# Kernel optimization log

Hardware: AMD Instinct MI355X
Metric: run time of the kernel (lower is better)

Reference implementation:

```python
import jax, jax.numpy as jnp
import numpy as np

B, N, C, HEADS, R = 8, 4096, 256, 8, 4  # N = H*W, R = reduction_ratio
LN_EPS = 1e-5


def setup_inputs() -> dict:
    key = jax.random.key(0)
    ks = jax.random.split(key, 6)
    sc = 0.02
    return {
        "x": jax.random.normal(ks[0], (B, N, C), jnp.float32),
        "conv_w": jax.random.normal(ks[1], (C, C, R, R), jnp.float32) * sc,  # OIHW
        "conv_b": jnp.zeros((C,), jnp.float32),
        "ln_g": jnp.ones((C,), jnp.float32),
        "ln_b": jnp.zeros((C,), jnp.float32),
        "kv_w": jax.random.normal(ks[2], (2 * C, C), jnp.float32) * sc,  # torch Linear (out,in)
        "kv_b": jnp.zeros((2 * C,), jnp.float32),
        "q_w": jax.random.normal(ks[3], (C, C), jnp.float32) * sc,
        "q_b": jnp.zeros((C,), jnp.float32),
        "out_w": jax.random.normal(ks[4], (C, C), jnp.float32) * sc,
        "out_b": jnp.zeros((C,), jnp.float32),
        "H": 64,
        "W": 64,
    }


def reference(x, conv_w, conv_b, ln_g, ln_b, kv_w, kv_b, q_w, q_b, out_w, out_b, H, W):
    Bz, Nq, Ch = x.shape
    d = Ch // HEADS
    scale = 1.0 / np.sqrt(float(d)).astype(np.float32)

    # spatial reduction: (B,N,C) -> (B,C,H,W) -> strided conv -> (B, M, C)
    x1 = x.transpose(0, 2, 1).reshape(Bz, Ch, H, W)
    x1 = jax.lax.conv_general_dilated(
        x1, conv_w, window_strides=(R, R), padding="VALID",
        dimension_numbers=("NCHW", "OIHW", "NCHW"))
    x1 = x1 + conv_b[None, :, None, None]
    x1 = x1.reshape(Bz, Ch, -1).transpose(0, 2, 1)  # (B, M, C), M=(H/R)*(W/R)

    # LayerNorm over channels
    mu = x1.mean(-1, keepdims=True)
    var = x1.var(-1, keepdims=True)
    x1 = (x1 - mu) / jnp.sqrt(var + LN_EPS) * ln_g + ln_b

    # K,V from reduced tokens
    kv = x1 @ kv_w.T + kv_b                                  # (B, M, 2C)
    M = kv.shape[1]
    kv = kv.reshape(Bz, M, 2, HEADS, d).transpose(2, 0, 3, 1, 4)  # (2,B,h,M,d)
    k, v = kv[0], kv[1]

    # Q from full-resolution tokens
    q = (x @ q_w.T + q_b).reshape(Bz, Nq, HEADS, d).transpose(0, 2, 1, 3)  # (B,h,N,d)

    attn = jax.nn.softmax(jnp.einsum("bhnd,bhmd->bhnm", q, k) * scale, axis=-1)
    out = jnp.einsum("bhnm,bhmd->bhnd", attn, v)             # (B,h,N,d)
    out = out.transpose(0, 2, 1, 3).reshape(Bz, Nq, Ch)
    return out @ out_w.T + out_b
```

## Files before the change

kernel.cpp:

```cpp
#include <hip/hip_runtime.h>
#include <math.h>

#define LN_EPS 1e-5f
#define SCALE_QK 0.17677669529663687f

using bf16x8 = __bf16 __attribute__((ext_vector_type(8)));
using f32x4 = float __attribute__((ext_vector_type(4)));

__device__ __forceinline__ ushort f2bf(float f) {
  unsigned u = __float_as_uint(f);
  u += 0x7fff + ((u >> 16) & 1);
  return (ushort)(u >> 16);
}

__device__ __forceinline__ void gload_lds16(const ushort* g, ushort* l) {
  __builtin_amdgcn_global_load_lds((__attribute__((address_space(1))) void*)g,
                                   (__attribute__((address_space(3))) void*)l, 16, 0, 0);
}

__global__ __launch_bounds__(256) void prep_kernel(
    const float* __restrict__ x, ushort* __restrict__ xb,
    const float* __restrict__ qw, const float* __restrict__ kvw,
    const float* __restrict__ ow, const float* __restrict__ cw,
    ushort* __restrict__ qwb, ushort* __restrict__ kvwb,
    ushort* __restrict__ owb, ushort* __restrict__ wTb) {
  int blk = blockIdx.x, tid = threadIdx.x;
  if (blk < 2048) {
    int i = blk * 1024 + tid;
#pragma unroll
    for (int p = 0; p < 4; ++p) {
      float4 v = ((const float4*)x)[i + p * 256];
      ushort4 o = {f2bf(v.x), f2bf(v.y), f2bf(v.z), f2bf(v.w)};
      ((ushort4*)xb)[i + p * 256] = o;
    }
  } else if (blk < 2304) {
    int b2 = blk - 2048;
    const float* src;
    ushort* dst;
    int i;
    if (b2 < 64) { src = qw; dst = qwb; i = b2 * 256 + tid; }
    else if (b2 < 192) { src = kvw; dst = kvwb; i = (b2 - 64) * 256 + tid; }
    else { src = ow; dst = owb; i = (b2 - 192) * 256 + tid; }
    float4 v = ((const float4*)src)[i];
    ushort4 o = {f2bf(v.x), f2bf(v.y), f2bf(v.z), f2bf(v.w)};
    ((ushort4*)dst)[i] = o;
  } else {
    int oc = blk - 2304, ic = tid;
    const float* src = cw + (size_t)oc * 4096 + ic * 16;
#pragma unroll
    for (int pos = 0; pos < 16; ++pos)
      wTb[(size_t)oc * 4096 + pos * 256 + ic] = f2bf(src[pos]);
  }
}

template <bool CONV, bool BIAS, int OUTMODE>
__global__ __launch_bounds__(256) void mfma_gemm(const ushort* __restrict__ A,
                                                 const ushort* __restrict__ Bw,
                                                 const float* __restrict__ bias,
                                                 float* __restrict__ C,
                                                 ushort* __restrict__ aux,
                                                 ushort* __restrict__ aux2, int Kld,
                                                 int Kslice, int Nld, size_t zstride) {
  __shared__ __attribute__((aligned(16))) ushort As[128 * 32];
  __shared__ __attribute__((aligned(16))) ushort Bs[64 * 32];
  int tid = threadIdx.x;
  int lane = tid & 63, w = tid >> 6;
  int m0 = blockIdx.y * 128, n0 = blockIdx.x * 64;
  int kbase = blockIdx.z * Kslice;
  int arow0 = w * 16 + (lane >> 2);
  int acol = (lane & 3) * 8;
  f32x4 acc[2][4];
#pragma unroll
  for (int i = 0; i < 2; ++i)
#pragma unroll
    for (int j = 0; j < 4; ++j) acc[i][j] = (f32x4){0.f, 0.f, 0.f, 0.f};

  for (int k0 = 0; k0 < Kslice; k0 += 32) {
    int kg = kbase + k0;
    __syncthreads();
#pragma unroll
    for (int t = 0; t < 2; ++t) {
      int row = arow0 + t * 64;
      const ushort* src;
      if (CONV) {
        int m = m0 + row;
        int b = m >> 8, mm = m & 255;
        int oh = mm >> 4, ow = mm & 15;
        int k = kg + acol;
        int pos = k >> 8, ic = k & 255;
        int n = ((oh << 2) + (pos >> 2)) * 64 + (ow << 2) + (pos & 3);
        src = A + ((size_t)(b * 4096 + n) * 256 + ic);
      } else {
        src = A + ((size_t)(m0 + row) * Kld + kg + acol);
      }
      gload_lds16(src, &As[t * 2048 + w * 512]);
    }
    {
      const ushort* srcb = Bw + ((size_t)(n0 + w * 16 + (lane >> 2)) * Kld + kg + acol);
      gload_lds16(srcb, &Bs[w * 512]);
    }
    __syncthreads();
    int qk = (lane >> 4) * 8, l15 = lane & 15;
    bf16x8 a0 = *(const bf16x8*)&As[(w * 32 + l15) * 32 + qk];
    bf16x8 a1 = *(const bf16x8*)&As[(w * 32 + 16 + l15) * 32 + qk];
#pragma unroll
    for (int j = 0; j < 4; ++j) {
      bf16x8 bj = *(const bf16x8*)&Bs[(j * 16 + l15) * 32 + qk];
      acc[0][j] = __builtin_amdgcn_mfma_f32_16x16x32_bf16(a0, bj, acc[0][j], 0, 0, 0);
      acc[1][j] = __builtin_amdgcn_mfma_f32_16x16x32_bf16(a1, bj, acc[1][j], 0, 0, 0);
    }
  }
  int l15 = lane & 15, q = lane >> 4;
  if (OUTMODE == 0) {
    float* Cz = C + (size_t)blockIdx.z * zstride;
#pragma unroll
    for (int i = 0; i < 2; ++i) {
#pragma unroll
      for (int j = 0; j < 4; ++j) {
        int col = n0 + j * 16 + l15;
        float bv = BIAS ? bias[col] : 0.f;
#pragma unroll
        for (int r = 0; r < 4; ++r) {
          int row = m0 + w * 32 + i * 16 + q * 4 + r;
          Cz[(size_t)row * Nld + col] = acc[i][j][r] + bv;
        }
      }
    }
  } else {
#pragma unroll
    for (int i = 0; i < 2; ++i) {
      int rowb = m0 + w * 32 + i * 16 + q * 4;
      int b = rowb >> 8, mloc = rowb & 255;
#pragma unroll
      for (int j = 0; j < 4; ++j) {
        int col = n0 + j * 16 + l15;
        float bv = bias[col];
        if (col < 256) {
#pragma unroll
          for (int r = 0; r < 4; ++r)
            aux[(size_t)(b * 256 + mloc + r) * 256 + col] = f2bf(acc[i][j][r] + bv);
        } else {
          int c2 = col - 256, h = c2 >> 5, d = c2 & 31;
          unsigned lo = (unsigned)f2bf(acc[i][j][0] + bv) |
                        ((unsigned)f2bf(acc[i][j][1] + bv) << 16);
          unsigned hi = (unsigned)f2bf(acc[i][j][2] + bv) |
                        ((unsigned)f2bf(acc[i][j][3] + bv) << 16);
          *(uint2*)(aux2 + ((size_t)((b * 8 + h) * 32 + d) * 256 + mloc)) =
              make_uint2(lo, hi);
        }
      }
    }
  }
}

template <bool F32OUT>
__global__ __launch_bounds__(256, 2) void breg_gemm(const ushort* __restrict__ A,
                                                    const ushort* __restrict__ Bw,
                                                    const float* __restrict__ bias,
                                                    float* __restrict__ Cf,
                                                    ushort* __restrict__ Cb) {
  int tid = threadIdx.x, lane = tid & 63, w = tid >> 6;
  int l15 = lane & 15, quad = lane >> 4;
  int n0 = blockIdx.x * 64;
  int m0 = blockIdx.y * 256 + w * 64;
  bf16x8 bfr[4][8];
  const ushort* bbase = Bw + (size_t)(n0 + l15) * 256 + quad * 8;
#pragma unroll
  for (int j = 0; j < 4; ++j)
#pragma unroll
    for (int kc = 0; kc < 8; ++kc)
      bfr[j][kc] = *(const bf16x8*)(bbase + (size_t)j * 16 * 256 + kc * 32);
  float bv[4];
#pragma unroll
  for (int j = 0; j < 4; ++j) bv[j] = bias[n0 + j * 16 + l15];

#pragma unroll
  for (int t = 0; t < 4; ++t) {
    const ushort* arow = A + (size_t)(m0 + t * 16 + l15) * 256 + quad * 8;
    bf16x8 af[8];
#pragma unroll
    for (int kc = 0; kc < 8; ++kc) af[kc] = *(const bf16x8*)(arow + kc * 32);
    f32x4 acc[4];
#pragma unroll
    for (int j = 0; j < 4; ++j) acc[j] = (f32x4){0.f, 0.f, 0.f, 0.f};
#pragma unroll
    for (int kc = 0; kc < 8; ++kc)
#pragma unroll
      for (int j = 0; j < 4; ++j)
        acc[j] = __builtin_amdgcn_mfma_f32_16x16x32_bf16(af[kc], bfr[j][kc], acc[j], 0, 0, 0);
#pragma unroll
    for (int j = 0; j < 4; ++j)
#pragma unroll
      for (int r = 0; r < 4; ++r) {
        int row = m0 + t * 16 + quad * 4 + r;
        int col = n0 + j * 16 + l15;
        float vv = acc[j][r] + bv[j];
        if (F32OUT) Cf[(size_t)row * 256 + col] = vv;
        else Cb[(size_t)row * 256 + col] = f2bf(vv);
      }
  }
}

__global__ __launch_bounds__(256) void ln_fused(const float* __restrict__ part,
                                                const float* __restrict__ cb,
                                                const float* __restrict__ g,
                                                const float* __restrict__ bt,
                                                ushort* __restrict__ x1b) {
  int t = blockIdx.x, c = threadIdx.x;
  size_t idx = (size_t)t * 256 + c;
  float v = cb[c];
#pragma unroll
  for (int z = 0; z < 8; ++z) v += part[idx + (size_t)z * 524288];
  float s1 = v, s2 = v * v;
#pragma unroll
  for (int o = 32; o > 0; o >>= 1) {
    s1 += __shfl_down(s1, o, 64);
    s2 += __shfl_down(s2, o, 64);
  }
  __shared__ float r1[4], r2[4];
  __shared__ float mu_s, rstd_s;
  int wv = c >> 6, lane = c & 63;
  if (lane == 0) { r1[wv] = s1; r2[wv] = s2; }
  __syncthreads();
  if (c == 0) {
    float S1 = r1[0] + r1[1] + r1[2] + r1[3];
    float S2 = r2[0] + r2[1] + r2[2] + r2[3];
    float mu = S1 * (1.f / 256.f);
    float var = S2 * (1.f / 256.f) - mu * mu;
    mu_s = mu;
    rstd_s = rsqrtf(var + LN_EPS);
  }
  __syncthreads();
  x1b[idx] = f2bf((v - mu_s) * rstd_s * g[c] + bt[c]);
}

__global__ __launch_bounds__(256) void attn_mfma(const ushort* __restrict__ qbb,
                                                 const ushort* __restrict__ kb,
                                                 const ushort* __restrict__ vT,
                                                 ushort* __restrict__ aob) {
  __shared__ __attribute__((aligned(16))) ushort sh[4 * 16 * 264];
  int bid = blockIdx.x;
  int chunk = bid & 15, h = (bid >> 4) & 7, b = bid >> 7;
  int tid = threadIdx.x, lane = tid & 63, w = tid >> 6;
  int l15 = lane & 15, quad = lane >> 4;

  {
    const ushort* srcK = kb + (size_t)(b * 256 + w * 64 + (lane >> 2)) * 256 +
                         h * 32 + (lane & 3) * 8;
#pragma unroll
    for (int i = 0; i < 4; ++i)
      gload_lds16(srcK + (size_t)i * 16 * 256, &sh[(w * 64 + i * 16) * 32]);
    const ushort* srcV = vT + (size_t)((b * 8 + h) * 32 + w * 8 + (lane >> 5)) * 256 +
                         (lane & 31) * 8;
#pragma unroll
    for (int i = 0; i < 4; ++i)
      gload_lds16(srcV + (size_t)i * 2 * 256, &sh[8192 + (w * 8 + i * 2) * 256]);
  }
  __syncthreads();
  bf16x8 kf[16];
#pragma unroll
  for (int mt = 0; mt < 16; ++mt)
    kf[mt] = *(const bf16x8*)&sh[(mt * 16 + l15) * 32 + quad * 8];
  bf16x8 vf[2][8];
#pragma unroll
  for (int j = 0; j < 2; ++j)
#pragma unroll
    for (int kc = 0; kc < 8; ++kc)
      vf[j][kc] = *(const bf16x8*)&sh[8192 + (j * 16 + l15) * 256 + kc * 32 + quad * 8];
  __syncthreads();
  ushort* Pw = &sh[w * 16 * 264];

  const float Cc = SCALE_QK * 1.4426950408889634f;
  int q0base = b * 4096 + chunk * 256 + w * 64;

  for (int t = 0; t < 4; ++t) {
    int q0 = q0base + t * 16;
    bf16x8 qf = *(const bf16x8*)(qbb + (size_t)(q0 + l15) * 256 + h * 32 + quad * 8);
    float lsum = 0.f;
#pragma unroll
    for (int mt = 0; mt < 16; ++mt) {
      f32x4 st = __builtin_amdgcn_mfma_f32_16x16x32_bf16(
          kf[mt], qf, (f32x4){0.f, 0.f, 0.f, 0.f}, 0, 0, 0);
      unsigned u[4];
#pragma unroll
      for (int r = 0; r < 4; ++r) {
        float e = __builtin_amdgcn_exp2f(st[r] * Cc);
        lsum += e;
        u[r] = __float_as_uint(e) + 0x8000u;
      }
      unsigned lo = (u[0] >> 16) | (u[1] & 0xffff0000u);
      unsigned hi = (u[2] >> 16) | (u[3] & 0xffff0000u);
      *(uint2*)(Pw + l15 * 264 + mt * 16 + quad * 4) = make_uint2(lo, hi);
    }
    lsum += __shfl_xor(lsum, 16, 64);
    lsum += __shfl_xor(lsum, 32, 64);
    __builtin_amdgcn_s_waitcnt(0xc07f);
    f32x4 oacc[2] = {{0.f, 0.f, 0.f, 0.f}, {0.f, 0.f, 0.f, 0.f}};
#pragma unroll
    for (int kc = 0; kc < 8; ++kc) {
      bf16x8 pf = *(const bf16x8*)(Pw + l15 * 264 + kc * 32 + quad * 8);
      oacc[0] = __builtin_amdgcn_mfma_f32_16x16x32_bf16(pf, vf[0][kc], oacc[0], 0, 0, 0);
      oacc[1] = __builtin_amdgcn_mfma_f32_16x16x32_bf16(pf, vf[1][kc], oacc[1], 0, 0, 0);
    }
    float linv[4];
#pragma unroll
    for (int r = 0; r < 4; ++r) linv[r] = 1.0f / __shfl(lsum, quad * 4 + r, 64);
    ushort* ob = aob + (size_t)q0 * 256 + h * 32;
#pragma unroll
    for (int j = 0; j < 2; ++j)
#pragma unroll
      for (int r = 0; r < 4; ++r) {
        unsigned uo = __float_as_uint(oacc[j][r] * linv[r]) + 0x8000u;
        ob[(size_t)(quad * 4 + r) * 256 + j * 16 + l15] = (ushort)(uo >> 16);
      }
  }
}

extern "C" void kernel_launch(void* const* d_in, const int* in_sizes, int n_in,
                              void* d_out, int out_size, void* d_ws, size_t ws_size,
                              hipStream_t stream) {
  const float* x = (const float*)d_in[0];
  const float* conv_w = (const float*)d_in[1];
  const float* conv_b = (const float*)d_in[2];
  const float* ln_g = (const float*)d_in[3];
  const float* ln_b = (const float*)d_in[4];
  const float* kv_w = (const float*)d_in[5];
  const float* kv_b = (const float*)d_in[6];
  const float* q_w = (const float*)d_in[7];
  const float* q_b = (const float*)d_in[8];
  const float* out_w = (const float*)d_in[9];
  const float* out_b = (const float*)d_in[10];

  ushort* xb = (ushort*)d_ws;
  ushort* wTb = xb + 8388608;
  ushort* qwb = wTb + 1048576;
  ushort* kvwb = qwb + 65536;
  ushort* owb = kvwb + 131072;
  ushort* x1b = owb + 65536;
  ushort* kb = x1b + 524288;
  ushort* vT = kb + 524288;
  ushort* aob = xb;
  float* part = (float*)d_out;
  ushort* qbb = (ushort*)((float*)d_out + 4194304);

  prep_kernel<<<2560, 256, 0, stream>>>(x, xb, q_w, kv_w, out_w, conv_w,
                                        qwb, kvwb, owb, wTb);
  mfma_gemm<true, false, 0><<<dim3(4, 16, 8), 256, 0, stream>>>(
      xb, wTb, nullptr, part, nullptr, nullptr, 4096, 512, 256, 524288);
  ln_fused<<<2048, 256, 0, stream>>>(part, conv_b, ln_g, ln_b, x1b);
  mfma_gemm<false, true, 2><<<dim3(8, 16, 1), 256, 0, stream>>>(
      x1b, kvwb, kv_b, nullptr, kb, vT, 256, 256, 512, 0);
  breg_gemm<false><<<dim3(4, 128), 256, 0, stream>>>(xb, qwb, q_b, nullptr, qbb);
  attn_mfma<<<1024, 256, 0, stream>>>(qbb, kb, vT, aob);
  breg_gemm<true><<<dim3(4, 128), 256, 0, stream>>>(aob, owb, out_b, (float*)d_out, nullptr);
}
```

Measured before the change: 208.7 us.

## Merge conv split-K and Q projection into one launch, halve attention grid

Merges the strided-conv GEMM, now split-K over 4 slices of 1024 instead of 8 of 512, and the Q projection GEMM into a single launch whose blocks branch by index. The goal is to cut launch overhead and let the two independent GEMMs overlap on the GPU. The LayerNorm reduction now sums 4 partials instead of 8. The attention kernel runs 512 blocks, each doing 8 query tiles, so the K/V staging into LDS and registers is amortised over more work. The exp-to-bf16 packing uses the hardware v_cvt_pk_bf16_f32 instruction. Fewer conv blocks give each one longer serial K loops, and the mixed-branch kernel may be limited by the register-heavy Q path.

```diff
diff --git a/kernel.cpp b/kernel.cpp
--- a/kernel.cpp
+++ b/kernel.cpp
@@ -11,6 +11,12 @@
   unsigned u = __float_as_uint(f);
   u += 0x7fff + ((u >> 16) & 1);
   return (ushort)(u >> 16);
+}
+
+__device__ __forceinline__ unsigned cvt_pk_bf16(float a, float b) {
+  unsigned r;
+  asm("v_cvt_pk_bf16_f32 %0, %1, %2" : "=v"(r) : "v"(a), "v"(b));
+  return r;
 }
 
 __device__ __forceinline__ void gload_lds16(const ushort* g, ushort* l) {
@@ -53,112 +59,111 @@
   }
 }
 
-template <bool CONV, bool BIAS, int OUTMODE>
-__global__ __launch_bounds__(256) void mfma_gemm(const ushort* __restrict__ A,
-                                                 const ushort* __restrict__ Bw,
-                                                 const float* __restrict__ bias,
-                                                 float* __restrict__ C,
-                                                 ushort* __restrict__ aux,
-                                                 ushort* __restrict__ aux2, int Kld,
-                                                 int Kslice, int Nld, size_t zstride) {
+__global__ __launch_bounds__(256, 2) void convq_kernel(
+    const ushort* __restrict__ xb, const ushort* __restrict__ wTb,
+    float* __restrict__ part, const ushort* __restrict__ qwb,
+    const float* __restrict__ qbias, ushort* __restrict__ qbb) {
   __shared__ __attribute__((aligned(16))) ushort As[128 * 32];
   __shared__ __attribute__((aligned(16))) ushort Bs[64 * 32];
-  int tid = threadIdx.x;
-  int lane = tid & 63, w = tid >> 6;
-  int m0 = blockIdx.y * 128, n0 = blockIdx.x * 64;
-  int kbase = blockIdx.z * Kslice;
-  int arow0 = w * 16 + (lane >> 2);
-  int acol = (lane & 3) * 8;
-  f32x4 acc[2][4];
-#pragma unroll
-  for (int i = 0; i < 2; ++i)
-#pragma unroll
-    for (int j = 0; j < 4; ++j) acc[i][j] = (f32x4){0.f, 0.f, 0.f, 0.f};
-
-  for (int k0 = 0; k0 < Kslice; k0 += 32) {
-    int kg = kbase + k0;
-    __syncthreads();
-#pragma unroll
-    for (int t = 0; t < 2; ++t) {
-      int row = arow0 + t * 64;
-      const ushort* src;
-      if (CONV) {
+  int tid = threadIdx.x, lane = tid & 63, w = tid >> 6;
+  int l15 = lane & 15, quad = lane >> 4;
+  int id = blockIdx.x;
+  if (id < 256) {
+    int n0 = (id & 3) * 64;
+    int m0 = ((id >> 2) & 15) * 128;
+    int bz = id >> 6;
+    int arow0 = w * 16 + (lane >> 2);
+    int acol = (lane & 3) * 8;
+    f32x4 acc[2][4];
+#pragma unroll
+    for (int i = 0; i < 2; ++i)
+#pragma unroll
+      for (int j = 0; j < 4; ++j) acc[i][j] = (f32x4){0.f, 0.f, 0.f, 0.f};
+
+    for (int k0 = 0; k0 < 1024; k0 += 32) {
+      int kg = bz * 1024 + k0;
+      __syncthreads();
+#pragma unroll
+      for (int t = 0; t < 2; ++t) {
+        int row = arow0 + t * 64;
         int m = m0 + row;
         int b = m >> 8, mm = m & 255;
-        int oh = mm >> 4, ow = mm & 15;
+        int oh = mm >> 4, ow_ = mm & 15;
         int k = kg + acol;
         int pos = k >> 8, ic = k & 255;
-        int n = ((oh << 2) + (pos >> 2)) * 64 + (ow << 2) + (pos & 3);
-        src = A + ((size_t)(b * 4096 + n) * 256 + ic);
-      } else {
-        src = A + ((size_t)(m0 + row) * Kld + kg + acol);
-      }
-      gload_lds16(src, &As[t * 2048 + w * 512]);
-    }
-    {
-      const ushort* srcb = Bw + ((size_t)(n0 + w * 16 + (lane >> 2)) * Kld + kg + acol);
-      gload_lds16(srcb, &Bs[w * 512]);
-    }
-    __syncthreads();
-    int qk = (lane >> 4) * 8, l15 = lane & 15;
-    bf16x8 a0 = *(const bf16x8*)&As[(w * 32 + l15) * 32 + qk];
-    bf16x8 a1 = *(const bf16x8*)&As[(w * 32 + 16 + l15) * 32 + qk];
-#pragma unroll
-    for (int j = 0; j < 4; ++j) {
-      bf16x8 bj = *(const bf16x8*)&Bs[(j * 16 + l15) * 32 + qk];
-      acc[0][j] = __builtin_amdgcn_mfma_f32_16x16x32_bf16(a0, bj, acc[0][j], 0, 0, 0);
-      acc[1][j] = __builtin_amdgcn_mfma_f32_16x16x32_bf16(a1, bj, acc[1][j], 0, 0, 0);
-    }
-  }
-  int l15 = lane & 15, q = lane >> 4;
-  if (OUTMODE == 0) {
-    float* Cz = C + (size_t)blockIdx.z * zstride;
-#pragma unroll
-    for (int i = 0; i < 2; ++i) {
+        int n = ((oh << 2) + (pos >> 2)) * 64 + (ow_ << 2) + (pos & 3);
+        gload_lds16(xb + ((size_t)(b * 4096 + n) * 256 + ic), &As[t * 2048 + w * 512]);
+      }
+      gload_lds16(wTb + ((size_t)(n0 + w * 16 + (lane >> 2)) * 4096 + kg + acol),
+                  &Bs[w * 512]);
+      __syncthreads();
+      int qk = quad * 8;
+      bf16x8 a0 = *(const bf16x8*)&As[(w * 32 + l15) * 32 + qk];
+      bf16x8 a1 = *(const bf16x8*)&As[(w * 32 + 16 + l15) * 32 + qk];
+#pragma unroll
+      for (int j = 0; j < 4; ++j) {
+        bf16x8 bj = *(const bf16x8*)&Bs[(j * 16 + l15) * 32 + qk];
+        acc[0][j] = __builtin_amdgcn_mfma_f32_16x16x32_bf16(a0, bj, acc[0][j], 0, 0, 0);
+        acc[1][j] = __builtin_amdgcn_mfma_f32_16x16x32_bf16(a1, bj, acc[1][j], 0, 0, 0);
+      }
+    }
+    float* Cz = part + (size_t)bz * 524288;
+#pragma unroll
+    for (int i = 0; i < 2; ++i)
 #pragma unroll
       for (int j = 0; j < 4; ++j) {
         int col = n0 + j * 16 + l15;
-        float bv = BIAS ? bias[col] : 0.f;
 #pragma unroll
         for (int r = 0; r < 4; ++r) {
-          int row = m0 + w * 32 + i * 16 + q * 4 + r;
-          Cz[(size_t)row * Nld + col] = acc[i][j][r] + bv;
+          int row = m0 + w * 32 + i * 16 + quad * 4 + r;
+          Cz[(size_t)row * 256 + col] = acc[i][j][r];
         }
       }
-    }
   } else {
-#pragma unroll
-    for (int i = 0; i < 2; ++i) {
-      int rowb = m0 + w * 32 + i * 16 + q * 4;
-      int b = rowb >> 8, mloc = rowb & 255;
-#pragma unroll
-      for (int j = 0; j < 4; ++j) {
-        int col = n0 + j * 16 + l15;
-        float bv = bias[col];
-        if (col < 256) {
-#pragma unroll
-          for (int r = 0; r < 4; ++r)
-            aux[(size_t)(b * 256 + mloc + r) * 256 + col] = f2bf(acc[i][j][r] + bv);
-        } else {
-          int c2 = col - 256, h = c2 >> 5, d = c2 & 31;
-          unsigned lo = (unsigned)f2bf(acc[i][j][0] + bv) |
-                        ((unsigned)f2bf(acc[i][j][1] + bv) << 16);
-          unsigned hi = (unsigned)f2bf(acc[i][j][2] + bv) |
-                        ((unsigned)f2bf(acc[i][j][3] + bv) << 16);
-          *(uint2*)(aux2 + ((size_t)((b * 8 + h) * 32 + d) * 256 + mloc)) =
-              make_uint2(lo, hi);
+    int qid = id - 256;
+    int n0 = (qid & 3) * 64;
+    int m0 = (qid >> 2) * 256 + w * 64;
+    bf16x8 bfr[4][8];
+    const ushort* bbase = qwb + (size_t)(n0 + l15) * 256 + quad * 8;
+#pragma unroll
+    for (int j = 0; j < 4; ++j)
+#pragma unroll
+      for (int kc = 0; kc < 8; ++kc)
+        bfr[j][kc] = *(const bf16x8*)(bbase + (size_t)j * 16 * 256 + kc * 32);
+    float bv[4];
+#pragma unroll
+    for (int j = 0; j < 4; ++j) bv[j] = qbias[n0 + j * 16 + l15];
+
+#pragma unroll
+    for (int t = 0; t < 4; ++t) {
+      const ushort* arow = xb + (size_t)(m0 + t * 16 + l15) * 256 + quad * 8;
+      bf16x8 af[8];
+#pragma unroll
+      for (int kc = 0; kc < 8; ++kc) af[kc] = *(const bf16x8*)(arow + kc * 32);
+      f32x4 acc[4];
+#pragma unroll
+      for (int j = 0; j < 4; ++j) acc[j] = (f32x4){0.f, 0.f, 0.f, 0.f};
+#pragma unroll
+      for (int kc = 0; kc < 8; ++kc)
+#pragma unroll
+        for (int j = 0; j < 4; ++j)
+          acc[j] = __builtin_amdgcn_mfma_f32_16x16x32_bf16(af[kc], bfr[j][kc], acc[j], 0, 0, 0);
+#pragma unroll
+      for (int j = 0; j < 4; ++j)
+#pragma unroll
+        for (int r = 0; r < 4; ++r) {
+          int row = m0 + t * 16 + quad * 4 + r;
+          int col = n0 + j * 16 + l15;
+          qbb[(size_t)row * 256 + col] = f2bf(acc[j][r] + bv[j]);
         }
-      }
-    }
-  }
-}
-
-template <bool F32OUT>
-__global__ __launch_bounds__(256, 2) void breg_gemm(const ushort* __restrict__ A,
-                                                    const ushort* __restrict__ Bw,
-                                                    const float* __restrict__ bias,
-                                                    float* __restrict__ Cf,
-                                                    ushort* __restrict__ Cb) {
+    }
+  }
+}
+
+__global__ __launch_bounds__(256, 2) void breg_gemm_f32(const ushort* __restrict__ A,
+                                                        const ushort* __restrict__ Bw,
+                                                        const float* __restrict__ bias,
+                                                        float* __restrict__ Cf) {
   int tid = threadIdx.x, lane = tid & 63, w = tid >> 6;
   int l15 = lane & 15, quad = lane >> 4;
   int n0 = blockIdx.x * 64;
@@ -194,9 +199,7 @@
       for (int r = 0; r < 4; ++r) {
         int row = m0 + t * 16 + quad * 4 + r;
         int col = n0 + j * 16 + l15;
-        float vv = acc[j][r] + bv[j];
-        if (F32OUT) Cf[(size_t)row * 256 + col] = vv;
-        else Cb[(size_t)row * 256 + col] = f2bf(vv);
+        Cf[(size_t)row * 256 + col] = acc[j][r] + bv[j];
       }
   }
 }
@@ -210,7 +213,7 @@
   size_t idx = (size_t)t * 256 + c;
   float v = cb[c];
 #pragma unroll
-  for (int z = 0; z < 8; ++z) v += part[idx + (size_t)z * 524288];
+  for (int z = 0; z < 4; ++z) v += part[idx + (size_t)z * 524288];
   float s1 = v, s2 = v * v;
 #pragma unroll
   for (int o = 32; o > 0; o >>= 1) {
@@ -234,13 +237,77 @@
   x1b[idx] = f2bf((v - mu_s) * rstd_s * g[c] + bt[c]);
 }
 
+__global__ __launch_bounds__(256) void kv_gemm(const ushort* __restrict__ A,
+                                               const ushort* __restrict__ Bw,
+                                               const float* __restrict__ bias,
+                                               ushort* __restrict__ aux,
+                                               ushort* __restrict__ aux2) {
+  __shared__ __attribute__((aligned(16))) ushort As[128 * 32];
+  __shared__ __attribute__((aligned(16))) ushort Bs[64 * 32];
+  int tid = threadIdx.x;
+  int lane = tid & 63, w = tid >> 6;
+  int m0 = blockIdx.y * 128, n0 = blockIdx.x * 64;
+  int arow0 = w * 16 + (lane >> 2);
+  int acol = (lane & 3) * 8;
+  f32x4 acc[2][4];
+#pragma unroll
+  for (int i = 0; i < 2; ++i)
+#pragma unroll
+    for (int j = 0; j < 4; ++j) acc[i][j] = (f32x4){0.f, 0.f, 0.f, 0.f};
+
+  for (int k0 = 0; k0 < 256; k0 += 32) {
+    __syncthreads();
+#pragma unroll
+    for (int t = 0; t < 2; ++t) {
+      int row = arow0 + t * 64;
+      gload_lds16(A + ((size_t)(m0 + row) * 256 + k0 + acol), &As[t * 2048 + w * 512]);
+    }
+    gload_lds16(Bw + ((size_t)(n0 + w * 16 + (lane >> 2)) * 256 + k0 + acol),
+                &Bs[w * 512]);
+    __syncthreads();
+    int qk = (lane >> 4) * 8, l15 = lane & 15;
+    bf16x8 a0 = *(const bf16x8*)&As[(w * 32 + l15) * 32 + qk];
+    bf16x8 a1 = *(const bf16x8*)&As[(w * 32 + 16 + l15) * 32 + qk];
+#pragma unroll
+    for (int j = 0; j < 4; ++j) {
+      bf16x8 bj = *(const bf16x8*)&Bs[(j * 16 + l15) * 32 + qk];
+      acc[0][j] = __builtin_amdgcn_mfma_f32_16x16x32_bf16(a0, bj, acc[0][j], 0, 0, 0);
+      acc[1][j] = __builtin_amdgcn_mfma_f32_16x16x32_bf16(a1, bj, acc[1][j], 0, 0, 0);
+    }
+  }
+  int l15 = lane & 15, q = lane >> 4;
+#pragma unroll
+  for (int i = 0; i < 2; ++i) {
+    int rowb = m0 + w * 32 + i * 16 + q * 4;
+    int b = rowb >> 8, mloc = rowb & 255;
+#pragma unroll
+    for (int j = 0; j < 4; ++j) {
+      int col = n0 + j * 16 + l15;
+      float bv = bias[col];
+      if (col < 256) {
+#pragma unroll
+        for (int r = 0; r < 4; ++r)
+          aux[(size_t)(b * 256 + mloc + r) * 256 + col] = f2bf(acc[i][j][r] + bv);
+      } else {
+        int c2 = col - 256, h = c2 >> 5, d = c2 & 31;
+        unsigned lo = (unsigned)f2bf(acc[i][j][0] + bv) |
+                      ((unsigned)f2bf(acc[i][j][1] + bv) << 16);
+        unsigned hi = (unsigned)f2bf(acc[i][j][2] + bv) |
+                      ((unsigned)f2bf(acc[i][j][3] + bv) << 16);
+        *(uint2*)(aux2 + ((size_t)((b * 8 + h) * 32 + d) * 256 + mloc)) =
+            make_uint2(lo, hi);
+      }
+    }
+  }
+}
+
 __global__ __launch_bounds__(256) void attn_mfma(const ushort* __restrict__ qbb,
                                                  const ushort* __restrict__ kb,
                                                  const ushort* __restrict__ vT,
                                                  ushort* __restrict__ aob) {
   __shared__ __attribute__((aligned(16))) ushort sh[4 * 16 * 264];
   int bid = blockIdx.x;
-  int chunk = bid & 15, h = (bid >> 4) & 7, b = bid >> 7;
+  int cp = bid & 7, h = (bid >> 3) & 7, b = bid >> 6;
   int tid = threadIdx.x, lane = tid & 63, w = tid >> 6;
   int l15 = lane & 15, quad = lane >> 4;
 
@@ -271,25 +338,23 @@
   ushort* Pw = &sh[w * 16 * 264];
 
   const float Cc = SCALE_QK * 1.4426950408889634f;
-  int q0base = b * 4096 + chunk * 256 + w * 64;
-
-  for (int t = 0; t < 4; ++t) {
-    int q0 = q0base + t * 16;
+  int q0base = b * 4096 + cp * 512 + w * 64;
+
+  for (int t = 0; t < 8; ++t) {
+    int q0 = q0base + ((t & 4) << 6) + (t & 3) * 16;
     bf16x8 qf = *(const bf16x8*)(qbb + (size_t)(q0 + l15) * 256 + h * 32 + quad * 8);
     float lsum = 0.f;
 #pragma unroll
     for (int mt = 0; mt < 16; ++mt) {
       f32x4 st = __builtin_amdgcn_mfma_f32_16x16x32_bf16(
           kf[mt], qf, (f32x4){0.f, 0.f, 0.f, 0.f}, 0, 0, 0);
-      unsigned u[4];
-#pragma unroll
-      for (int r = 0; r < 4; ++r) {
-        float e = __builtin_amdgcn_exp2f(st[r] * Cc);
-        lsum += e;
-        u[r] = __float_as_uint(e) + 0x8000u;
-      }
-      unsigned lo = (u[0] >> 16) | (u[1] & 0xffff0000u);
-      unsigned hi = (u[2] >> 16) | (u[3] & 0xffff0000u);
+      float e0 = __builtin_amdgcn_exp2f(st[0] * Cc);
+      float e1 = __builtin_amdgcn_exp2f(st[1] * Cc);
+      float e2 = __builtin_amdgcn_exp2f(st[2] * Cc);
+      float e3 = __builtin_amdgcn_exp2f(st[3] * Cc);
+      lsum += e0 + e1 + e2 + e3;
+      unsigned lo = cvt_pk_bf16(e0, e1);
+      unsigned hi = cvt_pk_bf16(e2, e3);
       *(uint2*)(Pw + l15 * 264 + mt * 16 + quad * 4) = make_uint2(lo, hi);
     }
     lsum += __shfl_xor(lsum, 16, 64);
@@ -345,12 +410,9 @@
 
   prep_kernel<<<2560, 256, 0, stream>>>(x, xb, q_w, kv_w, out_w, conv_w,
                                         qwb, kvwb, owb, wTb);
-  mfma_gemm<true, false, 0><<<dim3(4, 16, 8), 256, 0, stream>>>(
-      xb, wTb, nullptr, part, nullptr, nullptr, 4096, 512, 256, 524288);
+  convq_kernel<<<768, 256, 0, stream>>>(xb, wTb, part, qwb, q_b, qbb);
   ln_fused<<<2048, 256, 0, stream>>>(part, conv_b, ln_g, ln_b, x1b);
-  mfma_gemm<false, true, 2><<<dim3(8, 16, 1), 256, 0, stream>>>(
-      x1b, kvwb, kv_b, nullptr, kb, vT, 256, 256, 512, 0);
-  breg_gemm<false><<<dim3(4, 128), 256, 0, stream>>>(xb, qwb, q_b, nullptr, qbb);
-  attn_mfma<<<1024, 256, 0, stream>>>(qbb, kb, vT, aob);
-  breg_gemm<true><<<dim3(4, 128), 256, 0, stream>>>(aob, owb, out_b, (float*)d_out, nullptr);
-}
+  kv_gemm<<<dim3(8, 16), 256, 0, stream>>>(x1b, kvwb, kv_b, kb, vT);
+  attn_mfma<<<512, 256, 0, stream>>>(qbb, kb, vT, aob);
+  breg_gemm_f32<<<dim3(4, 128), 256, 0, stream>>>(aob, owb, out_b, (float*)d_out);
+}
```

New measurement: 195.0 us. -6.6%, faster.
